# Kernel optimization log

Hardware: AMD Instinct MI355X
Metric: run time of the kernel (lower is better)

Reference implementation:

```python
import jax, jax.numpy as jnp
import numpy as np

B, S, D, H = 2, 2048, 1024, 16
DK = D // H

def setup_inputs() -> dict:
    key = jax.random.key(0)
    ks = jax.random.split(key, 12)
    sc = 1.0 / np.sqrt(D)
    inp = {
        'query': jax.random.normal(ks[0], (B, S, D), jnp.float32),
        'key':   jax.random.normal(ks[1], (B, S, D), jnp.float32),
        'value': jax.random.normal(ks[2], (B, S, D), jnp.float32),
        'attn_mask': jnp.tril(jnp.ones((S, S), jnp.int32))[None, None],  # [1,1,S,S] causal
        'Wq': jax.random.normal(ks[3], (D, D), jnp.float32) * sc,
        'bq': jnp.zeros((D,), jnp.float32),
        'Wk': jax.random.normal(ks[4], (D, D), jnp.float32) * sc,
        'bk': jnp.zeros((D,), jnp.float32),
        'Wv': jax.random.normal(ks[5], (D, D), jnp.float32) * sc,
        'bv': jnp.zeros((D,), jnp.float32),
        'Wo': jax.random.normal(ks[6], (D, D), jnp.float32) * sc,
        'bo': jnp.zeros((D,), jnp.float32),
    }
    return inp

def reference(query, key, value, attn_mask, Wq, bq, Wk, bk, Wv, bv, Wo, bo):
    # QKV projections, split heads: [B,S,D] -> [B,H,S,DK]
    def proj(x, W, b):
        y = jnp.einsum('bsd,ed->bse', x, W) + b  # torch Linear: x @ W.T + b
        return y.reshape(B, S, H, DK).transpose(0, 2, 1, 3)
    q, k, v = proj(query, Wq, bq), proj(key, Wk, bk), proj(value, Wv, bv)
    scores = jnp.einsum('bhqd,bhkd->bhqk', q, k) / jnp.sqrt(jnp.float32(DK))
    scores = jnp.where(attn_mask == 0, jnp.float32(-1e9), scores)
    p_attn = jax.nn.softmax(scores, axis=-1)  # dropout = identity (eval)
    attn_outputs = jnp.einsum('bhqk,bhkd->bhqd', p_attn, v)  # [B,H,S,DK]
    # NOTE: module's quirk: 'attn_weights' is mean over d_k of the attended values
    attn_weights = jnp.mean(attn_outputs, axis=-1)  # [B,H,S]
    out = attn_outputs.transpose(0, 2, 1, 3).reshape(B, S, D)
    out = jnp.einsum('bsd,ed->bse', out, Wo) + bo
    return (out, attn_weights)
```

## Files before the change

kernel.cpp:

```cpp
#include <hip/hip_runtime.h>
#include <hip/hip_bf16.h>
#include <stdint.h>

#define B_ 2
#define S_ 2048
#define D_ 1024
#define H_ 16
#define DK_ 64
#define M_ 4096
#define K_ 1024

typedef unsigned short u16;
typedef u16   u16x4  __attribute__((ext_vector_type(4)));
typedef short short8 __attribute__((ext_vector_type(8)));
typedef float f32x4  __attribute__((ext_vector_type(4)));
typedef uint32_t u32x4 __attribute__((ext_vector_type(4)));

__device__ __forceinline__ u16 f2bf(float f) {
  uint32_t u = __builtin_bit_cast(uint32_t, f);
  u += 0x7FFFu + ((u >> 16) & 1u);
  return (u16)(u >> 16);
}

__device__ __forceinline__ uint32_t cvtpk(float lo, float hi) {
  uint32_t r;
  asm("v_cvt_pk_bf16_f32 %0, %1, %2" : "=v"(r) : "v"(lo), "v"(hi));
  return r;
}

__device__ __forceinline__ void gload_lds16(const void* g, void* l) {
  __builtin_amdgcn_global_load_lds(
      (const __attribute__((address_space(1))) void*)g,
      (__attribute__((address_space(3))) void*)l, 16, 0, 0);
}

__global__ __launch_bounds__(256) void cvt4w(const float* __restrict__ a,
                                             const float* __restrict__ b,
                                             const float* __restrict__ c,
                                             const float* __restrict__ d,
                                             u16* __restrict__ oa, u16* __restrict__ ob,
                                             u16* __restrict__ oc, u16* __restrict__ od) {
  const int z = blockIdx.y;
  const float* in = z == 0 ? a : (z == 1 ? b : (z == 2 ? c : d));
  u16* out = z == 0 ? oa : (z == 1 ? ob : (z == 2 ? oc : od));
  const int i = (blockIdx.x * 256 + threadIdx.x) * 4;
  const float4 v = *(const float4*)(in + i);
  u16x4 o;
  o[0] = f2bf(v.x); o[1] = f2bf(v.y); o[2] = f2bf(v.z); o[3] = f2bf(v.w);
  *(u16x4*)(out + i) = o;
}

__global__ __launch_bounds__(256) void gemm_qkv(
    const float* __restrict__ Aq, const float* __restrict__ Ak, const float* __restrict__ Av,
    const u16* __restrict__ Wqp, const u16* __restrict__ Wkp, const u16* __restrict__ Wvp,
    const float* __restrict__ bqp, const float* __restrict__ bkp, const float* __restrict__ bvp,
    u16* __restrict__ oq, u16* __restrict__ okk, u16* __restrict__ ov) {
  __shared__ float As[128 * 64];
  __shared__ u16  Bs[128 * 64];

  const int g = blockIdx.x;
  const int T = (g & 7) * 96 + (g >> 3);
  const int z = T >> 8;
  const int rem = T & 255;
  const int m0 = (rem >> 3) * 128, n0 = (rem & 7) * 128;

  const float* A    = z == 0 ? Aq  : (z == 1 ? Ak  : Av);
  const u16*   W    = z == 0 ? Wqp : (z == 1 ? Wkp : Wvp);
  const float* bias = z == 0 ? bqp : (z == 1 ? bkp : bvp);
  u16* out          = z == 0 ? oq  : (z == 1 ? okk : ov);
  const float scale = z == 0 ? 0.125f : 1.0f;

  const int tid = threadIdx.x;
  const int w = tid >> 6, lane = tid & 63;
  const int lr = lane & 15, lk = lane >> 4;
  const int wr = w >> 1, wc = w & 1;

  f32x4 acc[4][4] = {};

  const int arow   = w * 4 + (lane >> 4);
  const int acolsz = ((lane & 15) * 16) ^ ((arow & 7) << 4);
  const int trow   = tid >> 3;
  const int tcolsz = ((tid & 7) * 16) ^ ((trow & 7) << 4);
  const int rswz   = (lr & 7) << 4;
  const u16* Wbase = W + (size_t)(n0 + trow) * K_;

  for (int k0 = 0; k0 < K_; k0 += 64) {
#pragma unroll
    for (int i = 0; i < 8; ++i) {
      const char* ga = (const char*)(A + (size_t)(m0 + i * 16 + arow) * K_ + k0) + acolsz;
      gload_lds16(ga, (char*)As + i * 4096 + w * 1024);
    }
#pragma unroll
    for (int i = 0; i < 4; ++i) {
      const char* gb = (const char*)(Wbase + (size_t)(i * 32) * K_ + k0) + tcolsz;
      gload_lds16(gb, (char*)Bs + i * 4096 + w * 1024);
    }
    __syncthreads();
#pragma unroll
    for (int kk = 0; kk < 2; ++kk) {
      short8 af[4], bf[4];
#pragma unroll
      for (int mi = 0; mi < 4; ++mi) {
        const char* ap = (const char*)As + (wr * 64 + mi * 16 + lr) * 256;
        const f32x4 lo = *(const f32x4*)(ap + ((kk * 128 + lk * 32) ^ rswz));
        const f32x4 hi = *(const f32x4*)(ap + ((kk * 128 + lk * 32 + 16) ^ rswz));
        u32x4 pk;
        pk[0] = cvtpk(lo[0], lo[1]);
        pk[1] = cvtpk(lo[2], lo[3]);
        pk[2] = cvtpk(hi[0], hi[1]);
        pk[3] = cvtpk(hi[2], hi[3]);
        af[mi] = __builtin_bit_cast(short8, pk);
      }
#pragma unroll
      for (int nj = 0; nj < 4; ++nj)
        bf[nj] = *(const short8*)((const char*)Bs + (wc * 64 + nj * 16 + lr) * 128 +
                                  ((kk * 64 + lk * 16) ^ rswz));
#pragma unroll
      for (int mi = 0; mi < 4; ++mi)
#pragma unroll
        for (int nj = 0; nj < 4; ++nj)
          acc[mi][nj] = __builtin_amdgcn_mfma_f32_16x16x32_bf16(af[mi], bf[nj],
                                                                acc[mi][nj], 0, 0, 0);
    }
    __syncthreads();
  }

#pragma unroll
  for (int nj = 0; nj < 4; ++nj) {
    const int col = n0 + wc * 64 + nj * 16 + lr;
    const float bv = bias[col];
    const int h = col >> 6, dk = col & 63;
#pragma unroll
    for (int mi = 0; mi < 4; ++mi) {
#pragma unroll
      for (int r = 0; r < 4; ++r) {
        const int row = m0 + wr * 64 + mi * 16 + lk * 4 + r;
        const float val = (acc[mi][nj][r] + bv) * scale;
        const int b = row >> 11, s = row & 2047;
        if (z != 2)
          out[((size_t)(b * H_ + h) * S_ + s) * DK_ + dk] = f2bf(val);
        else
          out[((size_t)(b * H_ + h) * DK_ + dk) * S_ + s] = f2bf(val);
      }
    }
  }
}

__global__ __launch_bounds__(256) void gemm_out(const u16* __restrict__ A,
                                                const u16* __restrict__ W,
                                                const float* __restrict__ bias,
                                                float* __restrict__ out) {
  __shared__ u16 As[128 * 64];
  __shared__ u16 Bs[128 * 64];
  const int g = blockIdx.x;
  const int T = (g & 7) * 32 + (g >> 3);
  const int m0 = (T >> 3) * 128, n0 = (T & 7) * 128;

  const int tid = threadIdx.x;
  const int w = tid >> 6, lane = tid & 63;
  const int lr = lane & 15, lk = lane >> 4;
  const int wr = w >> 1, wc = w & 1;

  f32x4 acc[4][4] = {};

  const int trow   = tid >> 3;
  const int tcolsz = ((tid & 7) * 16) ^ ((trow & 7) << 4);
  const int rswz   = (lr & 7) << 4;
  const u16* Abase = A + (size_t)(m0 + trow) * K_;
  const u16* Wbase = W + (size_t)(n0 + trow) * K_;

  for (int k0 = 0; k0 < K_; k0 += 64) {
#pragma unroll
    for (int i = 0; i < 4; ++i) {
      const char* ga = (const char*)(Abase + (size_t)(i * 32) * K_ + k0) + tcolsz;
      gload_lds16(ga, (char*)As + i * 4096 + w * 1024);
      const char* gb = (const char*)(Wbase + (size_t)(i * 32) * K_ + k0) + tcolsz;
      gload_lds16(gb, (char*)Bs + i * 4096 + w * 1024);
    }
    __syncthreads();
#pragma unroll
    for (int kk = 0; kk < 2; ++kk) {
      short8 af[4], bf[4];
#pragma unroll
      for (int mi = 0; mi < 4; ++mi)
        af[mi] = *(const short8*)((const char*)As + (wr * 64 + mi * 16 + lr) * 128 +
                                  ((kk * 64 + lk * 16) ^ rswz));
#pragma unroll
      for (int nj = 0; nj < 4; ++nj)
        bf[nj] = *(const short8*)((const char*)Bs + (wc * 64 + nj * 16 + lr) * 128 +
                                  ((kk * 64 + lk * 16) ^ rswz));
#pragma unroll
      for (int mi = 0; mi < 4; ++mi)
#pragma unroll
        for (int nj = 0; nj < 4; ++nj)
          acc[mi][nj] = __builtin_amdgcn_mfma_f32_16x16x32_bf16(af[mi], bf[nj],
                                                                acc[mi][nj], 0, 0, 0);
    }
    __syncthreads();
  }

#pragma unroll
  for (int nj = 0; nj < 4; ++nj) {
    const int col = n0 + wc * 64 + nj * 16 + lr;
    const float bv = bias[col];
#pragma unroll
    for (int mi = 0; mi < 4; ++mi)
#pragma unroll
      for (int r = 0; r < 4; ++r) {
        const int row = m0 + wr * 64 + mi * 16 + lk * 4 + r;
        out[(size_t)row * D_ + col] = acc[mi][nj][r] + bv;
      }
  }
}

__global__ __launch_bounds__(256) void flash64(const u16* __restrict__ Qh,
                                               const u16* __restrict__ Kh,
                                               const u16* __restrict__ Vt,
                                               u16* __restrict__ O,
                                               float* __restrict__ AW) {
  __shared__ u16 Ks[2][64 * 64];
  __shared__ u16 Vs[2][64 * 64];
  __shared__ u16 Ps[64 * 64];
  const int tid = threadIdx.x;
  const int w = tid >> 6, lane = tid & 63;
  const int lr = lane & 15, lk = lane >> 4;
  const int bh = blockIdx.x;
  const int qt = (gridDim.y - 1) - blockIdx.y;
  const int q0 = qt * 64;
  const int b = bh >> 4, h = bh & 15;
  const int nt = qt + 1;

  const u16* Qg = Qh + ((size_t)bh * S_ + q0 + w * 16 + lr) * DK_;
  short8 qf[2];
  qf[0] = *(const short8*)(Qg + lk * 8);
  qf[1] = *(const short8*)(Qg + 32 + lk * 8);

  float mrow[4], lrow[4];
  f32x4 o[4] = {};
#pragma unroll
  for (int r = 0; r < 4; ++r) { mrow[r] = -__builtin_inff(); lrow[r] = 0.f; }

  const int trow = tid >> 3;
  const int tswz = ((tid & 7) * 16) ^ ((trow & 7) << 4);
  const int rswz = (lr & 7) << 4;
  const u16* Kgb = Kh + (size_t)bh * S_ * DK_;
  const u16* Vgb = Vt + (size_t)bh * DK_ * S_;

  auto STAGE = [&](int t, int d) {
    const int kv0 = t * 64;
#pragma unroll
    for (int i = 0; i < 2; ++i) {
      const char* gk = (const char*)(Kgb + (size_t)(kv0 + i * 32 + trow) * DK_) + tswz;
      gload_lds16(gk, (char*)Ks[d] + i * 4096 + w * 1024);
      const char* gv = (const char*)(Vgb + (size_t)(i * 32 + trow) * S_ + kv0) + tswz;
      gload_lds16(gv, (char*)Vs[d] + i * 4096 + w * 1024);
    }
  };

  STAGE(0, 0);
  __syncthreads();

  int cur = 0;
  for (int t = 0; t < nt; ++t) {
    if (t + 1 < nt) STAGE(t + 1, cur ^ 1);

    f32x4 sa[4] = {};
#pragma unroll
    for (int kk = 0; kk < 2; ++kk)
#pragma unroll
      for (int nj = 0; nj < 4; ++nj) {
        const short8 kf = *(const short8*)((const char*)Ks[cur] + (nj * 16 + lr) * 128 +
                                           ((kk * 64 + lk * 16) ^ rswz));
        sa[nj] = __builtin_amdgcn_mfma_f32_16x16x32_bf16(qf[kk], kf, sa[nj], 0, 0, 0);
      }

    if (t == qt) {
#pragma unroll
      for (int nj = 0; nj < 4; ++nj)
#pragma unroll
        for (int r = 0; r < 4; ++r)
          if (nj * 16 + lr > w * 16 + lk * 4 + r) sa[nj][r] = -1e30f;
    }

#pragma unroll
    for (int r = 0; r < 4; ++r) {
      float mx = fmaxf(fmaxf(sa[0][r], sa[1][r]), fmaxf(sa[2][r], sa[3][r]));
#pragma unroll
      for (int d = 1; d < 16; d <<= 1) mx = fmaxf(mx, __shfl_xor(mx, d));
      const float mn = fmaxf(mrow[r], mx);
      const float sc = __expf(mrow[r] - mn);
      mrow[r] = mn;
      float rs = 0.f;
#pragma unroll
      for (int nj = 0; nj < 4; ++nj) {
        const float p = __expf(sa[nj][r] - mn);
        sa[nj][r] = p;
        rs += p;
      }
      lrow[r] = lrow[r] * sc + rs;
#pragma unroll
      for (int nj = 0; nj < 4; ++nj) o[nj][r] *= sc;
    }

#pragma unroll
    for (int nj = 0; nj < 4; ++nj)
#pragma unroll
      for (int r = 0; r < 4; ++r) {
        const int rp = w * 16 + lk * 4 + r;
        *(u16*)((char*)Ps + rp * 128 + (((nj * 16 + lr) * 2) ^ ((rp & 7) << 4))) =
            f2bf(sa[nj][r]);
      }

#pragma unroll
    for (int kk = 0; kk < 2; ++kk) {
      const short8 pa = *(const short8*)((const char*)Ps + (w * 16 + lr) * 128 +
                                         ((kk * 64 + lk * 16) ^ rswz));
#pragma unroll
      for (int nj = 0; nj < 4; ++nj) {
        const short8 vf = *(const short8*)((const char*)Vs[cur] + (nj * 16 + lr) * 128 +
                                           ((kk * 64 + lk * 16) ^ rswz));
        o[nj] = __builtin_amdgcn_mfma_f32_16x16x32_bf16(pa, vf, o[nj], 0, 0, 0);
      }
    }
    __syncthreads();
    cur ^= 1;
  }

#pragma unroll
  for (int r = 0; r < 4; ++r) {
    float lt = lrow[r];
#pragma unroll
    for (int d = 1; d < 16; d <<= 1) lt += __shfl_xor(lt, d);
    const int rowq = q0 + w * 16 + lk * 4 + r;
    const float inv = 1.f / lt;
    float rsum = 0.f;
#pragma unroll
    for (int nj = 0; nj < 4; ++nj) {
      const float v = o[nj][r] * inv;
      O[((size_t)(b * S_ + rowq)) * D_ + h * 64 + nj * 16 + lr] = f2bf(v);
      rsum += v;
    }
#pragma unroll
    for (int d = 1; d < 16; d <<= 1) rsum += __shfl_xor(rsum, d);
    if (lr == 0) AW[(size_t)bh * S_ + rowq] = rsum * (1.f / 64.f);
  }
}

extern "C" void kernel_launch(void* const* d_in, const int* in_sizes, int n_in,
                              void* d_out, int out_size, void* d_ws, size_t ws_size,
                              hipStream_t stream) {
  const float* q  = (const float*)d_in[0];
  const float* k  = (const float*)d_in[1];
  const float* v  = (const float*)d_in[2];
  const float* Wq = (const float*)d_in[4];
  const float* bq = (const float*)d_in[5];
  const float* Wk = (const float*)d_in[6];
  const float* bk = (const float*)d_in[7];
  const float* Wv = (const float*)d_in[8];
  const float* bv = (const float*)d_in[9];
  const float* Wo = (const float*)d_in[10];
  const float* bo = (const float*)d_in[11];
  float* out = (float*)d_out;
  float* aw  = out + (size_t)M_ * D_;

  char* ws = (char*)d_ws;
  u16* Qh  = (u16*)(ws);
  u16* Kh  = (u16*)(ws + (8u << 20));
  u16* Vtb = (u16*)(ws + (16u << 20));
  u16* Ob  = (u16*)(ws + (24u << 20));
  u16* Wqb = (u16*)(ws + (32u << 20));
  u16* Wkb = (u16*)(ws + (34u << 20));
  u16* Wvb = (u16*)(ws + (36u << 20));
  u16* Wob = (u16*)(ws + (38u << 20));

  cvt4w<<<dim3(1024, 4), 256, 0, stream>>>(Wq, Wk, Wv, Wo, Wqb, Wkb, Wvb, Wob);

  gemm_qkv<<<768, 256, 0, stream>>>(q, k, v, Wqb, Wkb, Wvb,
                                    bq, bk, bv, Qh, Kh, Vtb);

  flash64<<<dim3(B_ * H_, S_ / 64), 256, 0, stream>>>(Qh, Kh, Vtb, Ob, aw);

  gemm_out<<<256, 256, 0, stream>>>(Ob, Wob, bo, out);
}
```

Before: 267.6 us.

## Double-buffer LDS tiles in QKV and output projection GEMMs with K=32 steps

```diff
diff --git a/kernel.cpp b/kernel.cpp
--- a/kernel.cpp
+++ b/kernel.cpp
@@ -55,8 +55,8 @@
     const u16* __restrict__ Wqp, const u16* __restrict__ Wkp, const u16* __restrict__ Wvp,
     const float* __restrict__ bqp, const float* __restrict__ bkp, const float* __restrict__ bvp,
     u16* __restrict__ oq, u16* __restrict__ okk, u16* __restrict__ ov) {
-  __shared__ float As[128 * 64];
-  __shared__ u16  Bs[128 * 64];
+  __shared__ float As[2][128 * 32];
+  __shared__ u16  Bs[2][128 * 32];
 
   const int g = blockIdx.x;
   const int T = (g & 7) * 96 + (g >> 3);
@@ -77,52 +77,58 @@
 
   f32x4 acc[4][4] = {};
 
-  const int arow   = w * 4 + (lane >> 4);
-  const int acolsz = ((lane & 15) * 16) ^ ((arow & 7) << 4);
-  const int trow   = tid >> 3;
-  const int tcolsz = ((tid & 7) * 16) ^ ((trow & 7) << 4);
-  const int rswz   = (lr & 7) << 4;
-  const u16* Wbase = W + (size_t)(n0 + trow) * K_;
-
-  for (int k0 = 0; k0 < K_; k0 += 64) {
-#pragma unroll
-    for (int i = 0; i < 8; ++i) {
-      const char* ga = (const char*)(A + (size_t)(m0 + i * 16 + arow) * K_ + k0) + acolsz;
-      gload_lds16(ga, (char*)As + i * 4096 + w * 1024);
-    }
-#pragma unroll
-    for (int i = 0; i < 4; ++i) {
-      const char* gb = (const char*)(Wbase + (size_t)(i * 32) * K_ + k0) + tcolsz;
-      gload_lds16(gb, (char*)Bs + i * 4096 + w * 1024);
-    }
+  const int arow   = tid >> 3;
+  const int acolsz = ((tid & 7) * 16) ^ ((arow & 7) << 4);
+  const int brow   = tid >> 2;
+  const int bcolsz = ((tid & 3) * 16) ^ ((brow & 3) << 4);
+  const int raswz  = (lr & 7) << 4;
+  const int rbswz  = (lr & 3) << 4;
+  const float* Ab = A + (size_t)(m0 + arow) * K_;
+  const u16*   Wb = W + (size_t)(n0 + brow) * K_;
+
+  auto STAGE = [&](int k0, int d) {
+#pragma unroll
+    for (int i = 0; i < 4; ++i)
+      gload_lds16((const char*)(Ab + (size_t)(i * 32) * K_ + k0) + acolsz,
+                  (char*)As[d] + i * 4096 + w * 1024);
+#pragma unroll
+    for (int i = 0; i < 2; ++i)
+      gload_lds16((const char*)(Wb + (size_t)(i * 64) * K_ + k0) + bcolsz,
+                  (char*)Bs[d] + i * 4096 + w * 1024);
+  };
+
+  STAGE(0, 0);
+  __syncthreads();
+
+  int cur = 0;
+  for (int t = 0; t < 32; ++t) {
+    if (t + 1 < 32) STAGE((t + 1) * 32, cur ^ 1);
+
+    short8 af[4], bf[4];
+#pragma unroll
+    for (int mi = 0; mi < 4; ++mi) {
+      const char* ap = (const char*)As[cur] + (wr * 64 + mi * 16 + lr) * 128;
+      const f32x4 lo = *(const f32x4*)(ap + ((lk * 32) ^ raswz));
+      const f32x4 hi = *(const f32x4*)(ap + ((lk * 32 + 16) ^ raswz));
+      u32x4 pk;
+      pk[0] = cvtpk(lo[0], lo[1]);
+      pk[1] = cvtpk(lo[2], lo[3]);
+      pk[2] = cvtpk(hi[0], hi[1]);
+      pk[3] = cvtpk(hi[2], hi[3]);
+      af[mi] = __builtin_bit_cast(short8, pk);
+    }
+#pragma unroll
+    for (int nj = 0; nj < 4; ++nj)
+      bf[nj] = *(const short8*)((const char*)Bs[cur] + (wc * 64 + nj * 16 + lr) * 64 +
+                                ((lk * 16) ^ rbswz));
+#pragma unroll
+    for (int mi = 0; mi < 4; ++mi)
+#pragma unroll
+      for (int nj = 0; nj < 4; ++nj)
+        acc[mi][nj] = __builtin_amdgcn_mfma_f32_16x16x32_bf16(af[mi], bf[nj],
+                                                              acc[mi][nj], 0, 0, 0);
     __syncthreads();
-#pragma unroll
-    for (int kk = 0; kk < 2; ++kk) {
-      short8 af[4], bf[4];
-#pragma unroll
-      for (int mi = 0; mi < 4; ++mi) {
-        const char* ap = (const char*)As + (wr * 64 + mi * 16 + lr) * 256;
-        const f32x4 lo = *(const f32x4*)(ap + ((kk * 128 + lk * 32) ^ rswz));
-        const f32x4 hi = *(const f32x4*)(ap + ((kk * 128 + lk * 32 + 16) ^ rswz));
-        u32x4 pk;
-        pk[0] = cvtpk(lo[0], lo[1]);
-        pk[1] = cvtpk(lo[2], lo[3]);
-        pk[2] = cvtpk(hi[0], hi[1]);
-        pk[3] = cvtpk(hi[2], hi[3]);
-        af[mi] = __builtin_bit_cast(short8, pk);
-      }
-#pragma unroll
-      for (int nj = 0; nj < 4; ++nj)
-        bf[nj] = *(const short8*)((const char*)Bs + (wc * 64 + nj * 16 + lr) * 128 +
-                                  ((kk * 64 + lk * 16) ^ rswz));
-#pragma unroll
-      for (int mi = 0; mi < 4; ++mi)
-#pragma unroll
-        for (int nj = 0; nj < 4; ++nj)
-          acc[mi][nj] = __builtin_amdgcn_mfma_f32_16x16x32_bf16(af[mi], bf[nj],
-                                                                acc[mi][nj], 0, 0, 0);
-    }
-    __syncthreads();
+    cur ^= 1;
   }
 
 #pragma unroll
@@ -150,8 +156,8 @@
                                                 const u16* __restrict__ W,
                                                 const float* __restrict__ bias,
                                                 float* __restrict__ out) {
-  __shared__ u16 As[128 * 64];
-  __shared__ u16 Bs[128 * 64];
+  __shared__ u16 As[2][128 * 32];
+  __shared__ u16 Bs[2][128 * 32];
   const int g = blockIdx.x;
   const int T = (g & 7) * 32 + (g >> 3);
   const int m0 = (T >> 3) * 128, n0 = (T & 7) * 128;
@@ -163,40 +169,46 @@
 
   f32x4 acc[4][4] = {};
 
-  const int trow   = tid >> 3;
-  const int tcolsz = ((tid & 7) * 16) ^ ((trow & 7) << 4);
-  const int rswz   = (lr & 7) << 4;
-  const u16* Abase = A + (size_t)(m0 + trow) * K_;
-  const u16* Wbase = W + (size_t)(n0 + trow) * K_;
-
-  for (int k0 = 0; k0 < K_; k0 += 64) {
-#pragma unroll
-    for (int i = 0; i < 4; ++i) {
-      const char* ga = (const char*)(Abase + (size_t)(i * 32) * K_ + k0) + tcolsz;
-      gload_lds16(ga, (char*)As + i * 4096 + w * 1024);
-      const char* gb = (const char*)(Wbase + (size_t)(i * 32) * K_ + k0) + tcolsz;
-      gload_lds16(gb, (char*)Bs + i * 4096 + w * 1024);
-    }
+  const int brow   = tid >> 2;
+  const int bcolsz = ((tid & 3) * 16) ^ ((brow & 3) << 4);
+  const int rbswz  = (lr & 3) << 4;
+  const u16* Abase = A + (size_t)(m0 + brow) * K_;
+  const u16* Wbase = W + (size_t)(n0 + brow) * K_;
+
+  auto STAGE = [&](int k0, int d) {
+#pragma unroll
+    for (int i = 0; i < 2; ++i) {
+      gload_lds16((const char*)(Abase + (size_t)(i * 64) * K_ + k0) + bcolsz,
+                  (char*)As[d] + i * 4096 + w * 1024);
+      gload_lds16((const char*)(Wbase + (size_t)(i * 64) * K_ + k0) + bcolsz,
+                  (char*)Bs[d] + i * 4096 + w * 1024);
+    }
+  };
+
+  STAGE(0, 0);
+  __syncthreads();
+
+  int cur = 0;
+  for (int t = 0; t < 32; ++t) {
+    if (t + 1 < 32) STAGE((t + 1) * 32, cur ^ 1);
+
+    short8 af[4], bf[4];
+#pragma unroll
+    for (int mi = 0; mi < 4; ++mi)
+      af[mi] = *(const short8*)((const char*)As[cur] + (wr * 64 + mi * 16 + lr) * 64 +
+                                ((lk * 16) ^ rbswz));
+#pragma unroll
+    for (int nj = 0; nj < 4; ++nj)
+      bf[nj] = *(const short8*)((const char*)Bs[cur] + (wc * 64 + nj * 16 + lr) * 64 +
+                                ((lk * 16) ^ rbswz));
+#pragma unroll
+    for (int mi = 0; mi < 4; ++mi)
+#pragma unroll
+      for (int nj = 0; nj < 4; ++nj)
+        acc[mi][nj] = __builtin_amdgcn_mfma_f32_16x16x32_bf16(af[mi], bf[nj],
+                                                              acc[mi][nj], 0, 0, 0);
     __syncthreads();
-#pragma unroll
-    for (int kk = 0; kk < 2; ++kk) {
-      short8 af[4], bf[4];
-#pragma unroll
-      for (int mi = 0; mi < 4; ++mi)
-        af[mi] = *(const short8*)((const char*)As + (wr * 64 + mi * 16 + lr) * 128 +
-                                  ((kk * 64 + lk * 16) ^ rswz));
-#pragma unroll
-      for (int nj = 0; nj < 4; ++nj)
-        bf[nj] = *(const short8*)((const char*)Bs + (wc * 64 + nj * 16 + lr) * 128 +
-                                  ((kk * 64 + lk * 16) ^ rswz));
-#pragma unroll
-      for (int mi = 0; mi < 4; ++mi)
-#pragma unroll
-        for (int nj = 0; nj < 4; ++nj)
-          acc[mi][nj] = __builtin_amdgcn_mfma_f32_16x16x32_bf16(af[mi], bf[nj],
-                                                                acc[mi][nj], 0, 0, 0);
-    }
-    __syncthreads();
+    cur ^= 1;
   }
 
 #pragma unroll
```

New measurement: 272.0 us. No clear change (+1.7%).
